# Kernel tuning notes

Measured on AMD Instinct MI355X. Metric: run time of the kernel, lower is better.

Reference implementation:

```python
import math
import jax, jax.numpy as jnp
import numpy as np

B, N, D = 8, 2048, 512


def setup_inputs() -> dict:
    key = jax.random.key(0)
    ks = jax.random.split(key, 9)
    s = 1.0 / math.sqrt(D)
    return {
        "x": jax.random.normal(ks[0], (B, N, D), dtype=jnp.float32),
        "adj": jax.random.uniform(ks[1], (B, N, N), dtype=jnp.float32),
        "Wqk": jax.random.normal(ks[2], (D, D), dtype=jnp.float32) * s,
        "bqk": jax.random.normal(ks[3], (D,), dtype=jnp.float32) * s,
        "Wl": jax.random.normal(ks[4], (D, D), dtype=jnp.float32) * s,
        "bl": jax.random.normal(ks[5], (D,), dtype=jnp.float32) * s,
        "Wr": jax.random.normal(ks[6], (D, D), dtype=jnp.float32) * s,
        "Wd": jax.random.normal(ks[7], (D, 1), dtype=jnp.float32),
        "bd": jax.random.normal(ks[8], (D,), dtype=jnp.float32),
    }


def reference(x, adj, Wqk, bqk, Wl, bl, Wr, Wd, bd):
    # degree gating: sigmoid(Linear(rowsum(adj)))
    deg = jnp.sum(adj, axis=-1, keepdims=True)           # [B, N, 1]
    gate = jax.nn.sigmoid(deg * Wd[:, 0] + bd)           # [B, N, D]
    xg = x * gate
    # sigmoid QK features
    QK = jax.nn.sigmoid(xg @ Wqk.T + bqk)                # [B, N, D]
    scores = jnp.einsum("bnd,bmd->bnm", QK, QK) / math.sqrt(D)
    scores = scores * adj                                # adjacency mask
    attn = scores / (jnp.sum(scores, axis=-1, keepdims=True) + 1e-6)
    out = jnp.einsum("bnm,bmd->bnd", attn, xg)           # aggregate values
    out = out @ Wl.T + bl + xg @ Wr.T                    # left + right branch
    return jax.nn.relu(out)
```

## Files before the change

kernel.cpp:

```cpp
#include <hip/hip_runtime.h>
#include <hip/hip_bf16.h>


typedef __bf16 bf16;
typedef __bf16 bf16x8 __attribute__((ext_vector_type(8)));
typedef float  f32x4  __attribute__((ext_vector_type(4)));

#define Bb 8
#define Nn 2048
#define Dd 512
#define SMEM_BYTES 33792

__device__ __forceinline__ bf16 to_bf16(float f) { return (bf16)f; }
__device__ __forceinline__ float sigmoidf_(float x) { return 1.0f / (1.0f + __expf(-x)); }

__device__ __forceinline__ void gld16(const void* g, void* l) {
    __builtin_amdgcn_global_load_lds(
        (__attribute__((address_space(1))) void*)(void*)g,
        (__attribute__((address_space(3))) void*)l,
        16, 0, 0);
}

__device__ __forceinline__ void gemm_bt_core(
    const bf16* __restrict__ A, const bf16* __restrict__ Bt,
    int lda, int ldb, int K,
    char* As, char* Bs, f32x4 acc[4][4])
{
    const int tid  = threadIdx.x;
    const int lane = tid & 63;
    const int wave = tid >> 6;
    const int wm = (wave >> 1) << 6;
    const int wn = (wave & 1) << 6;

    for (int kt = 0; kt < K; kt += 64) {
#pragma unroll
        for (int i = 0; i < 4; ++i) {
            int ff   = i * 256 + tid;
            int row  = ff >> 3;
            int slot = ff & 7;
            int gch  = slot ^ (row & 7);
            gld16(A  + (size_t)row * lda + kt + gch * 8, As + ff * 16);
            gld16(Bt + (size_t)row * ldb + kt + gch * 8, Bs + ff * 16);
        }
        __syncthreads();
#pragma unroll
        for (int ks = 0; ks < 2; ++ks) {
            bf16x8 af[4], bfr[4];
#pragma unroll
            for (int mi = 0; mi < 4; ++mi) {
                int row  = wm + mi * 16 + (lane & 15);
                int slot = ((ks << 2) + (lane >> 4)) ^ (row & 7);
                af[mi] = *(const bf16x8*)(As + row * 128 + slot * 16);
            }
#pragma unroll
            for (int ni = 0; ni < 4; ++ni) {
                int row  = wn + ni * 16 + (lane & 15);
                int slot = ((ks << 2) + (lane >> 4)) ^ (row & 7);
                bfr[ni] = *(const bf16x8*)(Bs + row * 128 + slot * 16);
            }
#pragma unroll
            for (int mi = 0; mi < 4; ++mi)
#pragma unroll
                for (int ni = 0; ni < 4; ++ni)
                    acc[mi][ni] = __builtin_amdgcn_mfma_f32_16x16x32_bf16(
                        af[mi], bfr[ni], acc[mi][ni], 0, 0, 0);
        }
        __syncthreads();
    }
}

#define GEMM_PROLOGUE()                                  \
    __shared__ __align__(16) char smem[SMEM_BYTES];      \
    char* As = smem;                                     \
    char* Bs = smem + 16384;                             \
    f32x4 acc[4][4];                                     \
    _Pragma("unroll") for (int mi = 0; mi < 4; ++mi)     \
    _Pragma("unroll") for (int ni = 0; ni < 4; ++ni)     \
        acc[mi][ni] = (f32x4){0.f, 0.f, 0.f, 0.f};

template <typename F>
__device__ __forceinline__ void epilogue_rt(f32x4 acc[4][4], char* smem, F&& emit)
{
    const int tid  = threadIdx.x;
    const int lane = tid & 63;
    const int wave = tid >> 6;
    const int wm = (wave >> 1) << 6;
    const int wn = (wave & 1) << 6;
    const int cq = lane >> 4;
    const int cl = lane & 15;
    float* t = (float*)smem;
    const int chunk = tid & 15;
    const int rbase = tid >> 4;
#pragma unroll
    for (int ph = 0; ph < 2; ++ph) {
        __syncthreads();
        if ((wm >> 6) == ph) {
#pragma unroll
            for (int mi = 0; mi < 4; ++mi)
#pragma unroll
                for (int ni = 0; ni < 4; ++ni)
#pragma unroll
                    for (int r = 0; r < 4; ++r) {
                        int lr = mi * 16 + cq * 4 + r;
                        int lc = wn + ni * 16 + cl;
                        t[lr * 132 + lc] = acc[mi][ni][r];
                    }
        }
        __syncthreads();
#pragma unroll
        for (int rr = 0; rr < 4; ++rr) {
            int lr = rr * 16 + rbase;
            f32x4 a = *(const f32x4*)&t[lr * 132 + chunk * 8];
            f32x4 b = *(const f32x4*)&t[lr * 132 + chunk * 8 + 4];
            float v[8] = {a[0], a[1], a[2], a[3], b[0], b[1], b[2], b[3]};
            emit(ph * 64 + lr, chunk * 8, v);
        }
    }
}

__global__ __launch_bounds__(256) void k_castw(
    const float* __restrict__ Wqk, const float* __restrict__ Wl,
    const float* __restrict__ Wr,
    bf16* __restrict__ Wqkb, bf16* __restrict__ Wlb, bf16* __restrict__ Wrb)
{
    int i = blockIdx.x * 256 + threadIdx.x;
    Wqkb[i] = to_bf16(Wqk[i]);
    Wlb[i]  = to_bf16(Wl[i]);
    Wrb[i]  = to_bf16(Wr[i]);
}

__global__ __launch_bounds__(256) void k_gate(
    const float* __restrict__ x, const float* __restrict__ adj,
    const float* __restrict__ Wd, const float* __restrict__ bd,
    bf16* __restrict__ xg)
{
    const int rowg = blockIdx.x;
    const float4* arow = (const float4*)(adj + (size_t)rowg * Nn);
    float4 v0 = arow[threadIdx.x];
    float4 v1 = arow[threadIdx.x + 256];
    float s = v0.x + v0.y + v0.z + v0.w + v1.x + v1.y + v1.z + v1.w;
#pragma unroll
    for (int off = 32; off > 0; off >>= 1) s += __shfl_down(s, off, 64);
    __shared__ float red[4];
    if ((threadIdx.x & 63) == 0) red[threadIdx.x >> 6] = s;
    __syncthreads();
    const float deg = red[0] + red[1] + red[2] + red[3];
#pragma unroll
    for (int d = threadIdx.x; d < Dd; d += 256) {
        float g = sigmoidf_(deg * Wd[d] + bd[d]);
        xg[(size_t)rowg * Dd + d] = to_bf16(x[(size_t)rowg * Dd + d] * g);
    }
}

__global__ __launch_bounds__(256) void k_transpose(
    const bf16* __restrict__ xg, bf16* __restrict__ xgT)
{
    const int b = blockIdx.z, nt = blockIdx.y, dt = blockIdx.x;
    __shared__ bf16 tile[64][66];
    const int c = threadIdx.x & 63, r0 = threadIdx.x >> 6;
    const bf16* src = xg + ((size_t)b * Nn + nt * 64) * Dd + dt * 64;
#pragma unroll
    for (int i = 0; i < 16; ++i) {
        int r = i * 4 + r0;
        tile[r][c] = src[(size_t)r * Dd + c];
    }
    __syncthreads();
    bf16* dst = xgT + ((size_t)b * Dd + dt * 64) * Nn + nt * 64;
#pragma unroll
    for (int i = 0; i < 16; ++i) {
        int r = i * 4 + r0;
        dst[(size_t)r * Nn + c] = tile[c][r];
    }
}

__global__ __launch_bounds__(256) void k_qk_gemm(
    const bf16* __restrict__ xg, const bf16* __restrict__ Wqkb,
    const float* __restrict__ bqk, bf16* __restrict__ QK)
{
    const int blockRow = blockIdx.y * 128;
    const int blockCol = blockIdx.x * 128;
    GEMM_PROLOGUE();
    gemm_bt_core(xg + (size_t)blockRow * Dd, Wqkb + (size_t)blockCol * Dd,
                 Dd, Dd, Dd, As, Bs, acc);
    epilogue_rt(acc, smem, [&](int lr, int lc, float* v) {
        int c = blockCol + lc;
        float4 b0 = *(const float4*)(bqk + c);
        float4 b1 = *(const float4*)(bqk + c + 4);
        float bb[8] = {b0.x, b0.y, b0.z, b0.w, b1.x, b1.y, b1.z, b1.w};
        bf16x8 o;
#pragma unroll
        for (int j = 0; j < 8; ++j) o[j] = to_bf16(sigmoidf_(v[j] + bb[j]));
        *(bf16x8*)(QK + (size_t)(blockRow + lr) * Dd + c) = o;
    });
}

__global__ __launch_bounds__(256) void k_s_gemm(
    const bf16* __restrict__ QK, const float* __restrict__ adj,
    bf16* __restrict__ S, float* __restrict__ denom)
{
    const int b = blockIdx.y;
    int t = blockIdx.x, i = 0;
    while (t >= 16 - i) { t -= 16 - i; ++i; }
    const int j = i + t;
    const int rowI = i * 128, rowJ = j * 128;
    const bf16* Qb = QK + (size_t)b * Nn * Dd;
    GEMM_PROLOGUE();
    gemm_bt_core(Qb + (size_t)rowI * Dd, Qb + (size_t)rowJ * Dd,
                 Dd, Dd, Dd, As, Bs, acc);
    const float scale = 0.044194173824159216f;

    const int tid  = threadIdx.x;
    const int lane = tid & 63;
    const int wave = tid >> 6;
    const int wm = (wave >> 1) << 6;
    const int wn = (wave & 1) << 6;
    const int cq = lane >> 4;
    const int cl = lane & 15;
    float* tls = (float*)smem;
    const int chunk = tid & 15;
    const int rbase = tid >> 4;

    auto store_side = [&](int blockRow, int blockCol, bool trans) {
#pragma unroll
        for (int ph = 0; ph < 2; ++ph) {
            __syncthreads();
            if (!trans) {
                if ((wave >> 1) == ph) {
#pragma unroll
                    for (int mi = 0; mi < 4; ++mi)
#pragma unroll
                        for (int ni = 0; ni < 4; ++ni)
#pragma unroll
                            for (int r = 0; r < 4; ++r)
                                tls[(mi * 16 + cq * 4 + r) * 132 + wn + ni * 16 + cl]
                                    = acc[mi][ni][r];
                }
            } else {
                if ((wave & 1) == ph) {
#pragma unroll
                    for (int mi = 0; mi < 4; ++mi)
#pragma unroll
                        for (int ni = 0; ni < 4; ++ni)
#pragma unroll
                            for (int r = 0; r < 4; ++r)
                                tls[(ni * 16 + cl) * 132 + wm + mi * 16 + cq * 4 + r]
                                    = acc[mi][ni][r];
                }
            }
            __syncthreads();
#pragma unroll
            for (int rr = 0; rr < 4; ++rr) {
                int lr = rr * 16 + rbase;
                f32x4 a = *(const f32x4*)&tls[lr * 132 + chunk * 8];
                f32x4 c4 = *(const f32x4*)&tls[lr * 132 + chunk * 8 + 4];
                float v[8] = {a[0], a[1], a[2], a[3], c4[0], c4[1], c4[2], c4[3]};
                int gRow = blockRow + ph * 64 + lr;
                size_t base = ((size_t)b * Nn + gRow) * Nn + blockCol + chunk * 8;
                float4 a0 = *(const float4*)(adj + base);
                float4 a1 = *(const float4*)(adj + base + 4);
                float aa[8] = {a0.x, a0.y, a0.z, a0.w, a1.x, a1.y, a1.z, a1.w};
                bf16x8 o;
                float ds = 0.f;
#pragma unroll
                for (int jj = 0; jj < 8; ++jj) {
                    float s = v[jj] * scale * aa[jj];
                    bf16 sb = to_bf16(s);
                    o[jj] = sb;
                    ds += (float)sb;
                }
                *(bf16x8*)(S + base) = o;
#pragma unroll
                for (int off = 8; off > 0; off >>= 1) ds += __shfl_xor(ds, off, 16);
                if ((tid & 15) == 0) atomicAdd(&denom[b * Nn + gRow], ds);
            }
        }
    };
    store_side(rowI, rowJ, false);
    if (i != j) store_side(rowJ, rowI, true);
}

__global__ __launch_bounds__(256) void k_h_gemm(
    const bf16* __restrict__ S, const bf16* __restrict__ xgT,
    const float* __restrict__ denom, bf16* __restrict__ h)
{
    const int id  = blockIdx.x;
    const int xcd = id & 7;
    const int pos = id >> 3;
    const int xt  = pos & 3;
    const int rg  = xcd * 16 + (pos >> 2);
    const int b   = rg >> 4;
    const int blockRow = (rg & 15) * 128;
    const int blockCol = xt * 128;
    GEMM_PROLOGUE();
    gemm_bt_core(S + ((size_t)b * Nn + blockRow) * Nn,
                 xgT + ((size_t)b * Dd + blockCol) * Nn,
                 Nn, Nn, Nn, As, Bs, acc);
    epilogue_rt(acc, smem, [&](int lr, int lc, float* v) {
        int gRow = blockRow + lr;
        float inv = 1.0f / (denom[b * Nn + gRow] + 1e-6f);
        bf16x8 o;
#pragma unroll
        for (int j = 0; j < 8; ++j) o[j] = to_bf16(v[j] * inv);
        *(bf16x8*)(h + ((size_t)b * Nn + gRow) * Dd + blockCol + lc) = o;
    });
}

__global__ __launch_bounds__(256) void k_out_gemm(
    const bf16* __restrict__ h, const bf16* __restrict__ xg,
    const bf16* __restrict__ Wlb, const bf16* __restrict__ Wrb,
    const float* __restrict__ bl, float* __restrict__ out)
{
    const int blockRow = blockIdx.y * 128;
    const int blockCol = blockIdx.x * 128;
    GEMM_PROLOGUE();
    gemm_bt_core(h  + (size_t)blockRow * Dd, Wlb + (size_t)blockCol * Dd,
                 Dd, Dd, Dd, As, Bs, acc);
    gemm_bt_core(xg + (size_t)blockRow * Dd, Wrb + (size_t)blockCol * Dd,
                 Dd, Dd, Dd, As, Bs, acc);
    epilogue_rt(acc, smem, [&](int lr, int lc, float* v) {
        int c = blockCol + lc;
        float4 b0 = *(const float4*)(bl + c);
        float4 b1 = *(const float4*)(bl + c + 4);
        float bb[8] = {b0.x, b0.y, b0.z, b0.w, b1.x, b1.y, b1.z, b1.w};
        float4 o0, o1;
        o0.x = fmaxf(v[0] + bb[0], 0.f); o0.y = fmaxf(v[1] + bb[1], 0.f);
        o0.z = fmaxf(v[2] + bb[2], 0.f); o0.w = fmaxf(v[3] + bb[3], 0.f);
        o1.x = fmaxf(v[4] + bb[4], 0.f); o1.y = fmaxf(v[5] + bb[5], 0.f);
        o1.z = fmaxf(v[6] + bb[6], 0.f); o1.w = fmaxf(v[7] + bb[7], 0.f);
        float* p = out + (size_t)(blockRow + lr) * Dd + c;
        *(float4*)p = o0;
        *(float4*)(p + 4) = o1;
    });
}

extern "C" void kernel_launch(void* const* d_in, const int* in_sizes, int n_in,
                              void* d_out, int out_size, void* d_ws, size_t ws_size,
                              hipStream_t stream) {
    const float* x   = (const float*)d_in[0];
    const float* adj = (const float*)d_in[1];
    const float* Wqk = (const float*)d_in[2];
    const float* bqk = (const float*)d_in[3];
    const float* Wl  = (const float*)d_in[4];
    const float* bl  = (const float*)d_in[5];
    const float* Wr  = (const float*)d_in[6];
    const float* Wd  = (const float*)d_in[7];
    const float* bd  = (const float*)d_in[8];
    float* out = (float*)d_out;

    char* ws = (char*)d_ws;
    bf16* xg   = (bf16*)ws;  ws += (size_t)Bb * Nn * Dd * 2;
    bf16* xgT  = (bf16*)ws;  ws += (size_t)Bb * Dd * Nn * 2;
    bf16* QK   = (bf16*)ws;  ws += (size_t)Bb * Nn * Dd * 2;
    bf16* S    = (bf16*)ws;  ws += (size_t)Bb * Nn * Nn * 2;
    bf16* Wqkb = (bf16*)ws;  ws += (size_t)Dd * Dd * 2;
    bf16* Wlb  = (bf16*)ws;  ws += (size_t)Dd * Dd * 2;
    bf16* Wrb  = (bf16*)ws;  ws += (size_t)Dd * Dd * 2;
    float* denom = (float*)ws; ws += (size_t)Bb * Nn * 4;
    bf16* h = QK;

    hipMemsetAsync(denom, 0, (size_t)Bb * Nn * sizeof(float), stream);
    k_castw<<<dim3(1024), 256, 0, stream>>>(Wqk, Wl, Wr, Wqkb, Wlb, Wrb);
    k_gate<<<dim3(Bb * Nn), 256, 0, stream>>>(x, adj, Wd, bd, xg);
    k_transpose<<<dim3(Dd / 64, Nn / 64, Bb), 256, 0, stream>>>(xg, xgT);
    k_qk_gemm<<<dim3(Dd / 128, (Bb * Nn) / 128), 256, 0, stream>>>(xg, Wqkb, bqk, QK);
    k_s_gemm<<<dim3(136, Bb), 256, 0, stream>>>(QK, adj, S, denom);
    k_h_gemm<<<dim3(512), 256, 0, stream>>>(S, xgT, denom, h);
    k_out_gemm<<<dim3(Dd / 128, (Bb * Nn) / 128), 256, 0, stream>>>(h, xg, Wlb, Wrb, bl, out);
}
```

Before: 388.9 us.

## Pre-cast adjacency to bf16 in gate kernel and drop LDS row padding

```diff
diff --git a/kernel.cpp b/kernel.cpp
--- a/kernel.cpp
+++ b/kernel.cpp
@@ -3,13 +3,15 @@
 
 
 typedef __bf16 bf16;
+typedef __bf16 bf16x2 __attribute__((ext_vector_type(2)));
+typedef __bf16 bf16x4 __attribute__((ext_vector_type(4)));
 typedef __bf16 bf16x8 __attribute__((ext_vector_type(8)));
 typedef float  f32x4  __attribute__((ext_vector_type(4)));
 
 #define Bb 8
 #define Nn 2048
 #define Dd 512
-#define SMEM_BYTES 33792
+#define SMEM_BYTES 32768
 
 __device__ __forceinline__ bf16 to_bf16(float f) { return (bf16)f; }
 __device__ __forceinline__ float sigmoidf_(float x) { return 1.0f / (1.0f + __expf(-x)); }
@@ -84,7 +86,6 @@
     const int tid  = threadIdx.x;
     const int lane = tid & 63;
     const int wave = tid >> 6;
-    const int wm = (wave >> 1) << 6;
     const int wn = (wave & 1) << 6;
     const int cq = lane >> 4;
     const int cl = lane & 15;
@@ -94,7 +95,7 @@
 #pragma unroll
     for (int ph = 0; ph < 2; ++ph) {
         __syncthreads();
-        if ((wm >> 6) == ph) {
+        if ((wave >> 1) == ph) {
 #pragma unroll
             for (int mi = 0; mi < 4; ++mi)
 #pragma unroll
@@ -103,15 +104,15 @@
                     for (int r = 0; r < 4; ++r) {
                         int lr = mi * 16 + cq * 4 + r;
                         int lc = wn + ni * 16 + cl;
-                        t[lr * 132 + lc] = acc[mi][ni][r];
+                        t[lr * 128 + lc] = acc[mi][ni][r];
                     }
         }
         __syncthreads();
 #pragma unroll
         for (int rr = 0; rr < 4; ++rr) {
             int lr = rr * 16 + rbase;
-            f32x4 a = *(const f32x4*)&t[lr * 132 + chunk * 8];
-            f32x4 b = *(const f32x4*)&t[lr * 132 + chunk * 8 + 4];
+            f32x4 a = *(const f32x4*)&t[lr * 128 + chunk * 8];
+            f32x4 b = *(const f32x4*)&t[lr * 128 + chunk * 8 + 4];
             float v[8] = {a[0], a[1], a[2], a[3], b[0], b[1], b[2], b[3]};
             emit(ph * 64 + lr, chunk * 8, v);
         }
@@ -132,24 +133,32 @@
 __global__ __launch_bounds__(256) void k_gate(
     const float* __restrict__ x, const float* __restrict__ adj,
     const float* __restrict__ Wd, const float* __restrict__ bd,
-    bf16* __restrict__ xg)
+    bf16* __restrict__ xg, bf16* __restrict__ adjb)
 {
     const int rowg = blockIdx.x;
+    const int tid = threadIdx.x;
     const float4* arow = (const float4*)(adj + (size_t)rowg * Nn);
-    float4 v0 = arow[threadIdx.x];
-    float4 v1 = arow[threadIdx.x + 256];
+    float4 v0 = arow[tid];
+    float4 v1 = arow[tid + 256];
+    bf16* ab = adjb + (size_t)rowg * Nn;
+    bf16x4 a0 = { to_bf16(v0.x), to_bf16(v0.y), to_bf16(v0.z), to_bf16(v0.w) };
+    bf16x4 a1 = { to_bf16(v1.x), to_bf16(v1.y), to_bf16(v1.z), to_bf16(v1.w) };
+    *(bf16x4*)(ab + tid * 4) = a0;
+    *(bf16x4*)(ab + 1024 + tid * 4) = a1;
     float s = v0.x + v0.y + v0.z + v0.w + v1.x + v1.y + v1.z + v1.w;
 #pragma unroll
     for (int off = 32; off > 0; off >>= 1) s += __shfl_down(s, off, 64);
     __shared__ float red[4];
-    if ((threadIdx.x & 63) == 0) red[threadIdx.x >> 6] = s;
+    if ((tid & 63) == 0) red[tid >> 6] = s;
     __syncthreads();
     const float deg = red[0] + red[1] + red[2] + red[3];
-#pragma unroll
-    for (int d = threadIdx.x; d < Dd; d += 256) {
-        float g = sigmoidf_(deg * Wd[d] + bd[d]);
-        xg[(size_t)rowg * Dd + d] = to_bf16(x[(size_t)rowg * Dd + d] * g);
-    }
+    float2 xv = ((const float2*)(x + (size_t)rowg * Dd))[tid];
+    float2 wv = ((const float2*)Wd)[tid];
+    float2 bv = ((const float2*)bd)[tid];
+    bf16x2 o;
+    o[0] = to_bf16(xv.x * sigmoidf_(deg * wv.x + bv.x));
+    o[1] = to_bf16(xv.y * sigmoidf_(deg * wv.y + bv.y));
+    *(bf16x2*)(xg + (size_t)rowg * Dd + tid * 2) = o;
 }
 
 __global__ __launch_bounds__(256) void k_transpose(
@@ -195,7 +204,7 @@
 }
 
 __global__ __launch_bounds__(256) void k_s_gemm(
-    const bf16* __restrict__ QK, const float* __restrict__ adj,
+    const bf16* __restrict__ QK, const bf16* __restrict__ adjb,
     bf16* __restrict__ S, float* __restrict__ denom)
 {
     const int b = blockIdx.y;
@@ -232,7 +241,7 @@
                         for (int ni = 0; ni < 4; ++ni)
 #pragma unroll
                             for (int r = 0; r < 4; ++r)
-                                tls[(mi * 16 + cq * 4 + r) * 132 + wn + ni * 16 + cl]
+                                tls[(mi * 16 + cq * 4 + r) * 128 + wn + ni * 16 + cl]
                                     = acc[mi][ni][r];
                 }
             } else {
@@ -241,29 +250,25 @@
                     for (int mi = 0; mi < 4; ++mi)
 #pragma unroll
                         for (int ni = 0; ni < 4; ++ni)
-#pragma unroll
-                            for (int r = 0; r < 4; ++r)
-                                tls[(ni * 16 + cl) * 132 + wm + mi * 16 + cq * 4 + r]
-                                    = acc[mi][ni][r];
+                            *(f32x4*)&tls[(ni * 16 + cl) * 128 + wm + mi * 16 + cq * 4]
+                                = acc[mi][ni];
                 }
             }
             __syncthreads();
 #pragma unroll
             for (int rr = 0; rr < 4; ++rr) {
                 int lr = rr * 16 + rbase;
-                f32x4 a = *(const f32x4*)&tls[lr * 132 + chunk * 8];
-                f32x4 c4 = *(const f32x4*)&tls[lr * 132 + chunk * 8 + 4];
+                f32x4 a = *(const f32x4*)&tls[lr * 128 + chunk * 8];
+                f32x4 c4 = *(const f32x4*)&tls[lr * 128 + chunk * 8 + 4];
                 float v[8] = {a[0], a[1], a[2], a[3], c4[0], c4[1], c4[2], c4[3]};
                 int gRow = blockRow + ph * 64 + lr;
                 size_t base = ((size_t)b * Nn + gRow) * Nn + blockCol + chunk * 8;
-                float4 a0 = *(const float4*)(adj + base);
-                float4 a1 = *(const float4*)(adj + base + 4);
-                float aa[8] = {a0.x, a0.y, a0.z, a0.w, a1.x, a1.y, a1.z, a1.w};
+                bf16x8 av = *(const bf16x8*)(adjb + base);
                 bf16x8 o;
                 float ds = 0.f;
 #pragma unroll
                 for (int jj = 0; jj < 8; ++jj) {
-                    float s = v[jj] * scale * aa[jj];
+                    float s = v[jj] * scale * (float)av[jj];
                     bf16 sb = to_bf16(s);
                     o[jj] = sb;
                     ds += (float)sb;
@@ -352,6 +357,7 @@
     bf16* xgT  = (bf16*)ws;  ws += (size_t)Bb * Dd * Nn * 2;
     bf16* QK   = (bf16*)ws;  ws += (size_t)Bb * Nn * Dd * 2;
     bf16* S    = (bf16*)ws;  ws += (size_t)Bb * Nn * Nn * 2;
+    bf16* adjb = (bf16*)ws;  ws += (size_t)Bb * Nn * Nn * 2;
     bf16* Wqkb = (bf16*)ws;  ws += (size_t)Dd * Dd * 2;
     bf16* Wlb  = (bf16*)ws;  ws += (size_t)Dd * Dd * 2;
     bf16* Wrb  = (bf16*)ws;  ws += (size_t)Dd * Dd * 2;
@@ -360,10 +366,10 @@
 
     hipMemsetAsync(denom, 0, (size_t)Bb * Nn * sizeof(float), stream);
     k_castw<<<dim3(1024), 256, 0, stream>>>(Wqk, Wl, Wr, Wqkb, Wlb, Wrb);
-    k_gate<<<dim3(Bb * Nn), 256, 0, stream>>>(x, adj, Wd, bd, xg);
+    k_gate<<<dim3(Bb * Nn), 256, 0, stream>>>(x, adj, Wd, bd, xg, adjb);
     k_transpose<<<dim3(Dd / 64, Nn / 64, Bb), 256, 0, stream>>>(xg, xgT);
     k_qk_gemm<<<dim3(Dd / 128, (Bb * Nn) / 128), 256, 0, stream>>>(xg, Wqkb, bqk, QK);
-    k_s_gemm<<<dim3(136, Bb), 256, 0, stream>>>(QK, adj, S, denom);
+    k_s_gemm<<<dim3(136, Bb), 256, 0, stream>>>(QK, adjb, S, denom);
     k_h_gemm<<<dim3(512), 256, 0, stream>>>(S, xgT, denom, h);
     k_out_gemm<<<dim3(Dd / 128, (Bb * Nn) / 128), 256, 0, stream>>>(h, xg, Wlb, Wrb, bl, out);
 }
```

New measurement: 409.9 us. 5.4% more time.
